# Optimization experiments

Hardware: AMD Instinct MI355X
Metric: run time of the kernel (lower is better)

Reference implementation:

```python
import jax, jax.numpy as jnp
import numpy as np

BATCH = 1024
SEQ = 80
VOCAB = 50000
EMB = 512
UNITS = 512


def setup_inputs() -> dict:
    key = jax.random.key(0)
    ks = jax.random.split(key, 10)
    s_in = 1.0 / np.sqrt(EMB)
    s_h = 1.0 / np.sqrt(UNITS)
    return {
        "inputs": jax.random.randint(ks[0], (BATCH, SEQ), 0, VOCAB, dtype=jnp.int64),
        "emb": jax.random.normal(ks[1], (VOCAB, EMB), dtype=jnp.float32) * 0.05,
        "W0x": jax.random.normal(ks[2], (EMB, UNITS), dtype=jnp.float32) * s_in,
        "W0h": jax.random.normal(ks[3], (UNITS, UNITS), dtype=jnp.float32) * s_h,
        "b0": jnp.zeros((UNITS,), dtype=jnp.float32),
        "W1x": jax.random.normal(ks[4], (UNITS, UNITS), dtype=jnp.float32) * s_h,
        "W1h": jax.random.normal(ks[5], (UNITS, UNITS), dtype=jnp.float32) * s_h,
        "b1": jnp.zeros((UNITS,), dtype=jnp.float32),
        "Wout": jax.random.normal(ks[6], (UNITS, 1), dtype=jnp.float32) * s_h,
        "bout": jnp.zeros((1,), dtype=jnp.float32),
    }


def reference(inputs, emb, W0x, W0h, b0, W1x, W1h, b1, Wout, bout):
    # Embedding lookup: [B, T, E]
    x = emb[inputs]
    # Time-major for scan: [T, B, E]
    xs = jnp.transpose(x, (1, 0, 2))

    h0 = jnp.zeros((inputs.shape[0], W0h.shape[0]), dtype=emb.dtype)
    h1 = jnp.zeros((inputs.shape[0], W1h.shape[0]), dtype=emb.dtype)

    def step(carry, x_t):
        h0, h1 = carry
        # SimpleRNNCell 0: tanh(x@Wx + h@Wh + b)  (dropout inactive at inference)
        h0 = jnp.tanh(x_t @ W0x + h0 @ W0h + b0)
        # SimpleRNNCell 1 stacked on cell 0's output
        h1 = jnp.tanh(h0 @ W1x + h1 @ W1h + b1)
        return (h0, h1), None

    (h0, h1), _ = jax.lax.scan(step, (h0, h1), xs)
    # Dense(1) on last-step hidden of layer 1, then sigmoid -> [B, 1]
    prob = jax.nn.sigmoid(h1 @ Wout + bout)
    return prob
```

## Files before the change

kernel.cpp:

```cpp
#include <hip/hip_runtime.h>
#include <hip/hip_bf16.h>
#include <math.h>

#define BATCH   1024
#define SEQ     80
#define EMB     512
#define UNITS   512
#define NBG     64
#define NCG     4
#define ROWS    16
#define COLS    128
#define THREADS 512
#define LDW     1544

#define H0_OFF   (2u * 1024 * 1024)
#define H1_OFF   (4u * 1024 * 1024)
#define FLAG_OFF (6u * 1024 * 1024)

typedef __attribute__((ext_vector_type(8))) short          bf16x8;
typedef __attribute__((ext_vector_type(8))) unsigned short u16x8;
typedef __attribute__((ext_vector_type(4))) float          f32x4;

__device__ inline unsigned short f2bf(float f) {
    __hip_bfloat16 h = __float2bfloat16(f);
    return *reinterpret_cast<unsigned short*>(&h);
}
__device__ inline float bf2f(unsigned short u) {
    unsigned int x = ((unsigned int)u) << 16;
    return __uint_as_float(x);
}
__device__ inline float tanh_fast(float x) {
    float e = __expf(2.f * x);
    return 1.f - 2.f / (e + 1.f);
}

__global__ __launch_bounds__(256) void pack_weights(
    const float* __restrict__ W0x, const float* __restrict__ W0h,
    const float* __restrict__ W1x, const float* __restrict__ W1h,
    unsigned short* __restrict__ wpack)
{
    int g    = blockIdx.x * 4 + (threadIdx.x >> 6);
    int lane = threadIdx.x & 63;
    int p    = g >> 10;
    int cg   = (g >> 8) & 3;
    int w    = (g >> 5) & 7;
    int k0   = g & 31;
    int n    = cg * COLS + w * 16 + (lane & 15);
    int kb   = k0 * 32 + (lane >> 4) * 8;
    const float* Wx = p ? W1x : W0x;
    const float* Wh = p ? W1h : W0h;

    u16x8 v;
#pragma unroll
    for (int j = 0; j < 8; ++j) {
        int k = kb + j;
        float f = (k < 512) ? Wx[(size_t)k * UNITS + n]
                            : Wh[(size_t)(k - 512) * UNITS + n];
        v[j] = f2bf(f);
    }
    *(u16x8*)(wpack + (size_t)g * 512 + lane * 8) = v;
}

#define RUN_PHASE(ACC, KBASE, WB)                                              \
    do {                                                                       \
        const unsigned short* a_lds = hcat + abase + (KBASE);                  \
        bf16x8 Bf[8];                                                          \
        _Pragma("unroll")                                                      \
        for (int i = 0; i < 8; ++i)                                            \
            Bf[i] = *(const bf16x8*)((WB) + (size_t)i * 512);                  \
        _Pragma("unroll")                                                      \
        for (int k0 = 0; k0 < 32; ++k0) {                                      \
            bf16x8 a = *(const bf16x8*)(a_lds + k0 * 32);                      \
            bf16x8 b = Bf[k0 & 7];                                             \
            if (k0 + 8 < 32)                                                   \
                Bf[k0 & 7] = *(const bf16x8*)((WB) + (size_t)(k0 + 8) * 512);  \
            ACC = __builtin_amdgcn_mfma_f32_16x16x32_bf16(a, b, ACC, 0, 0, 0); \
        }                                                                      \
    } while (0)

__global__ __launch_bounds__(THREADS, 1) void rnn_ex_kernel(
    const int*   __restrict__ inputs,
    const float* __restrict__ emb,
    const float* __restrict__ b0,
    const float* __restrict__ b1,
    const unsigned short* __restrict__ wpack,
    unsigned short* __restrict__ h0buf,
    unsigned short* __restrict__ h1buf,
    int* __restrict__ flag0,
    int* __restrict__ flag1,
    const float* __restrict__ Wout,
    const float* __restrict__ bout,
    float*       __restrict__ out)
{
    __shared__ unsigned short hcat[ROWS * LDW];

    const int tid   = threadIdx.x;
    const int w     = tid >> 6;
    const int lane  = tid & 63;
    const int quad  = lane >> 4;
    const int l15   = lane & 15;
    const int cg    = blockIdx.x >> 6;
    const int bg    = blockIdx.x & 63;
    const int rbase = bg * ROWS;

    for (int i = tid; i < ROWS * 1024; i += THREADS) {
        int r = i >> 10, c = i & 1023;
        hcat[r * LDW + 512 + c] = 0;
    }

    const int xr = tid >> 5;
    const int xc = (tid & 31) * 16;

    {
        int idx = inputs[(rbase + xr) * SEQ + 0];
        const float4* ep = (const float4*)(emb + (size_t)idx * EMB + xc);
        float4 p0 = ep[0], p1 = ep[1], p2 = ep[2], p3 = ep[3];
        u16x8 v0, v1;
        v0[0]=f2bf(p0.x); v0[1]=f2bf(p0.y); v0[2]=f2bf(p0.z); v0[3]=f2bf(p0.w);
        v0[4]=f2bf(p1.x); v0[5]=f2bf(p1.y); v0[6]=f2bf(p1.z); v0[7]=f2bf(p1.w);
        v1[0]=f2bf(p2.x); v1[1]=f2bf(p2.y); v1[2]=f2bf(p2.z); v1[3]=f2bf(p2.w);
        v1[4]=f2bf(p3.x); v1[5]=f2bf(p3.y); v1[6]=f2bf(p3.z); v1[7]=f2bf(p3.w);
        *(u16x8*)(hcat + xr * LDW + xc)     = v0;
        *(u16x8*)(hcat + xr * LDW + xc + 8) = v1;
    }
    __syncthreads();

    const int   mycol = cg * COLS + w * 16 + l15;
    const float bias0 = b0[mycol];
    const float bias1 = b1[mycol];

    const unsigned short* wb0 = wpack + ((size_t)(cg * 256 + w * 32)) * 512 + lane * 8;
    const unsigned short* wb1 = wb0 + (size_t)1024 * 512;

    const int abase = l15 * LDW + quad * 8;
    const int fl    = bg * NCG;

    for (int t = 0; t < SEQ; ++t) {
        const int par = t & 1;
        const int tgt = t + 1;

        int tn = (t + 1 < SEQ) ? t + 1 : t;
        int idx = inputs[(rbase + xr) * SEQ + tn];
        const float4* ep = (const float4*)(emb + (size_t)idx * EMB + xc);
        float4 p0 = ep[0], p1 = ep[1], p2 = ep[2], p3 = ep[3];

        f32x4 acc = {bias0, bias0, bias0, bias0};
        RUN_PHASE(acc, 0, wb0);
        {
            unsigned short* dst = h0buf +
                ((size_t)par * BATCH + rbase + quad * 4) * UNITS + mycol;
#pragma unroll
            for (int i = 0; i < 4; ++i)
                __hip_atomic_store(dst + (size_t)i * UNITS,
                                   f2bf(tanh_fast(acc[i])),
                                   __ATOMIC_RELAXED, __HIP_MEMORY_SCOPE_AGENT);
        }
        __syncthreads();
        if (tid == 0)
            __hip_atomic_store(&flag0[fl + cg], tgt,
                               __ATOMIC_RELEASE, __HIP_MEMORY_SCOPE_AGENT);
        if (tid < NCG)
            while (__hip_atomic_load(&flag0[fl + tid],
                                     __ATOMIC_RELAXED, __HIP_MEMORY_SCOPE_AGENT) < tgt)
                __builtin_amdgcn_s_sleep(1);
        __asm__ volatile("" ::: "memory");
        __syncthreads();
        {
            const unsigned long long* src = (const unsigned long long*)
                (h0buf + ((size_t)par * BATCH + rbase) * UNITS);
            int base = (xr * 512 + xc) >> 2;
            unsigned long long q0 = __hip_atomic_load(src + base + 0, __ATOMIC_RELAXED, __HIP_MEMORY_SCOPE_AGENT);
            unsigned long long q1 = __hip_atomic_load(src + base + 1, __ATOMIC_RELAXED, __HIP_MEMORY_SCOPE_AGENT);
            unsigned long long q2 = __hip_atomic_load(src + base + 2, __ATOMIC_RELAXED, __HIP_MEMORY_SCOPE_AGENT);
            unsigned long long q3 = __hip_atomic_load(src + base + 3, __ATOMIC_RELAXED, __HIP_MEMORY_SCOPE_AGENT);
            unsigned long long* d = (unsigned long long*)&hcat[xr * LDW + 512 + xc];
            d[0] = q0; d[1] = q1; d[2] = q2; d[3] = q3;

            u16x8 v0, v1;
            v0[0]=f2bf(p0.x); v0[1]=f2bf(p0.y); v0[2]=f2bf(p0.z); v0[3]=f2bf(p0.w);
            v0[4]=f2bf(p1.x); v0[5]=f2bf(p1.y); v0[6]=f2bf(p1.z); v0[7]=f2bf(p1.w);
            v1[0]=f2bf(p2.x); v1[1]=f2bf(p2.y); v1[2]=f2bf(p2.z); v1[3]=f2bf(p2.w);
            v1[4]=f2bf(p3.x); v1[5]=f2bf(p3.y); v1[6]=f2bf(p3.z); v1[7]=f2bf(p3.w);
            *(u16x8*)(hcat + xr * LDW + xc)     = v0;
            *(u16x8*)(hcat + xr * LDW + xc + 8) = v1;
        }
        __syncthreads();

        f32x4 acc2 = {bias1, bias1, bias1, bias1};
        RUN_PHASE(acc2, 512, wb1);
        {
            unsigned short* dst = h1buf +
                ((size_t)par * BATCH + rbase + quad * 4) * UNITS + mycol;
#pragma unroll
            for (int i = 0; i < 4; ++i)
                __hip_atomic_store(dst + (size_t)i * UNITS,
                                   f2bf(tanh_fast(acc2[i])),
                                   __ATOMIC_RELAXED, __HIP_MEMORY_SCOPE_AGENT);
        }
        __syncthreads();
        if (tid == 0)
            __hip_atomic_store(&flag1[fl + cg], tgt,
                               __ATOMIC_RELEASE, __HIP_MEMORY_SCOPE_AGENT);
        if (tid < NCG)
            while (__hip_atomic_load(&flag1[fl + tid],
                                     __ATOMIC_RELAXED, __HIP_MEMORY_SCOPE_AGENT) < tgt)
                __builtin_amdgcn_s_sleep(1);
        __asm__ volatile("" ::: "memory");
        __syncthreads();
        {
            const unsigned long long* src = (const unsigned long long*)
                (h1buf + ((size_t)par * BATCH + rbase) * UNITS);
            int base = (xr * 512 + xc) >> 2;
            unsigned long long q0 = __hip_atomic_load(src + base + 0, __ATOMIC_RELAXED, __HIP_MEMORY_SCOPE_AGENT);
            unsigned long long q1 = __hip_atomic_load(src + base + 1, __ATOMIC_RELAXED, __HIP_MEMORY_SCOPE_AGENT);
            unsigned long long q2 = __hip_atomic_load(src + base + 2, __ATOMIC_RELAXED, __HIP_MEMORY_SCOPE_AGENT);
            unsigned long long q3 = __hip_atomic_load(src + base + 3, __ATOMIC_RELAXED, __HIP_MEMORY_SCOPE_AGENT);
            unsigned long long* d = (unsigned long long*)&hcat[xr * LDW + 1024 + xc];
            d[0] = q0; d[1] = q1; d[2] = q2; d[3] = q3;
        }
    }
    __syncthreads();

    if (cg == 0) {
#pragma unroll
        for (int rr = 0; rr < 2; ++rr) {
            int r = w * 2 + rr;
            float s = 0.f;
#pragma unroll
            for (int j = 0; j < 8; ++j) {
                int c = lane + 64 * j;
                s += bf2f(hcat[r * LDW + 1024 + c]) * Wout[c];
            }
#pragma unroll
            for (int off = 32; off > 0; off >>= 1) s += __shfl_down(s, off);
            if (lane == 0) {
                float z = s + bout[0];
                out[rbase + r] = 1.f / (1.f + __expf(-z));
            }
        }
    }
}

extern "C" void kernel_launch(void* const* d_in, const int* in_sizes, int n_in,
                              void* d_out, int out_size, void* d_ws, size_t ws_size,
                              hipStream_t stream) {
    const int*   inputs = (const int*)d_in[0];
    const float* emb    = (const float*)d_in[1];
    const float* W0x    = (const float*)d_in[2];
    const float* W0h    = (const float*)d_in[3];
    const float* b0     = (const float*)d_in[4];
    const float* W1x    = (const float*)d_in[5];
    const float* W1h    = (const float*)d_in[6];
    const float* b1     = (const float*)d_in[7];
    const float* Wout   = (const float*)d_in[8];
    const float* bout   = (const float*)d_in[9];
    float*       out    = (float*)d_out;

    unsigned short* wpack = (unsigned short*)d_ws;
    unsigned short* h0buf = (unsigned short*)((char*)d_ws + H0_OFF);
    unsigned short* h1buf = (unsigned short*)((char*)d_ws + H1_OFF);
    int* flag0 = (int*)((char*)d_ws + FLAG_OFF);
    int* flag1 = flag0 + 256;

    hipMemsetAsync((char*)d_ws + FLAG_OFF, 0, 2048, stream);
    pack_weights<<<512, 256, 0, stream>>>(W0x, W0h, W1x, W1h, wpack);
    rnn_ex_kernel<<<NBG * NCG, THREADS, 0, stream>>>(
        inputs, emb, b0, b1, wpack, h0buf, h1buf, flag0, flag1,
        Wout, bout, out);
}
```

Baseline: 1.103 ms.

## Overlap input-side GEMM halves with cross-block waits and keep recurrent weights in registers

Splits each layer's K=1024 GEMM into an input half and a recurrent half. The halves that do not depend on the freshly exchanged hidden state (x@W0x for the next step, h1_prev@W1h) are computed while waiting on the inter-block flags, so only the dependent half sits on the critical path. The dependent-half weights (W0h and W1x) are preloaded once into registers, removing global weight loads from the critical path. The embedding and state copies are also remapped to 16-byte accesses. This raises register pressure with 256 extra VGPRs of weights per thread, which risks spills under the 512-thread launch bound.

```diff
diff --git a/kernel.cpp b/kernel.cpp
--- a/kernel.cpp
+++ b/kernel.cpp
@@ -17,9 +17,10 @@
 #define H1_OFF   (4u * 1024 * 1024)
 #define FLAG_OFF (6u * 1024 * 1024)
 
-typedef __attribute__((ext_vector_type(8))) short          bf16x8;
-typedef __attribute__((ext_vector_type(8))) unsigned short u16x8;
-typedef __attribute__((ext_vector_type(4))) float          f32x4;
+typedef __attribute__((ext_vector_type(8))) short              bf16x8;
+typedef __attribute__((ext_vector_type(8))) unsigned short     u16x8;
+typedef __attribute__((ext_vector_type(4))) float              f32x4;
+typedef __attribute__((ext_vector_type(2))) unsigned long long u64x2;
 
 __device__ inline unsigned short f2bf(float f) {
     __hip_bfloat16 h = __float2bfloat16(f);
@@ -32,6 +33,12 @@
 __device__ inline float tanh_fast(float x) {
     float e = __expf(2.f * x);
     return 1.f - 2.f / (e + 1.f);
+}
+__device__ inline u16x8 pack8(float4 p0, float4 p1) {
+    u16x8 v;
+    v[0]=f2bf(p0.x); v[1]=f2bf(p0.y); v[2]=f2bf(p0.z); v[3]=f2bf(p0.w);
+    v[4]=f2bf(p1.x); v[5]=f2bf(p1.y); v[6]=f2bf(p1.z); v[7]=f2bf(p1.w);
+    return v;
 }
 
 __global__ __launch_bounds__(256) void pack_weights(
@@ -61,7 +68,7 @@
     *(u16x8*)(wpack + (size_t)g * 512 + lane * 8) = v;
 }
 
-#define RUN_PHASE(ACC, KBASE, WB)                                              \
+#define RUN_HALF_STREAM(ACC, KBASE, WB)                                        \
     do {                                                                       \
         const unsigned short* a_lds = hcat + abase + (KBASE);                  \
         bf16x8 Bf[8];                                                          \
@@ -69,12 +76,22 @@
         for (int i = 0; i < 8; ++i)                                            \
             Bf[i] = *(const bf16x8*)((WB) + (size_t)i * 512);                  \
         _Pragma("unroll")                                                      \
-        for (int k0 = 0; k0 < 32; ++k0) {                                      \
+        for (int k0 = 0; k0 < 16; ++k0) {                                      \
             bf16x8 a = *(const bf16x8*)(a_lds + k0 * 32);                      \
             bf16x8 b = Bf[k0 & 7];                                             \
-            if (k0 + 8 < 32)                                                   \
+            if (k0 + 8 < 16)                                                   \
                 Bf[k0 & 7] = *(const bf16x8*)((WB) + (size_t)(k0 + 8) * 512);  \
             ACC = __builtin_amdgcn_mfma_f32_16x16x32_bf16(a, b, ACC, 0, 0, 0); \
+        }                                                                      \
+    } while (0)
+
+#define RUN_HALF_REG(ACC, KBASE, BR)                                           \
+    do {                                                                       \
+        const unsigned short* a_lds = hcat + abase + (KBASE);                  \
+        _Pragma("unroll")                                                      \
+        for (int k0 = 0; k0 < 16; ++k0) {                                      \
+            bf16x8 a = *(const bf16x8*)(a_lds + k0 * 32);                      \
+            ACC = __builtin_amdgcn_mfma_f32_16x16x32_bf16(a, (BR)[k0], ACC, 0, 0, 0); \
         }                                                                      \
     } while (0)
 
@@ -92,7 +109,7 @@
     const float* __restrict__ bout,
     float*       __restrict__ out)
 {
-    __shared__ unsigned short hcat[ROWS * LDW];
+    __shared__ __align__(16) unsigned short hcat[ROWS * LDW];
 
     const int tid   = threadIdx.x;
     const int w     = tid >> 6;
@@ -103,25 +120,22 @@
     const int bg    = blockIdx.x & 63;
     const int rbase = bg * ROWS;
 
+    const int gr = w;
+    const int gc = (tid & 63) * 8;
+
     for (int i = tid; i < ROWS * 1024; i += THREADS) {
         int r = i >> 10, c = i & 1023;
         hcat[r * LDW + 512 + c] = 0;
     }
 
-    const int xr = tid >> 5;
-    const int xc = (tid & 31) * 16;
-
     {
-        int idx = inputs[(rbase + xr) * SEQ + 0];
-        const float4* ep = (const float4*)(emb + (size_t)idx * EMB + xc);
-        float4 p0 = ep[0], p1 = ep[1], p2 = ep[2], p3 = ep[3];
-        u16x8 v0, v1;
-        v0[0]=f2bf(p0.x); v0[1]=f2bf(p0.y); v0[2]=f2bf(p0.z); v0[3]=f2bf(p0.w);
-        v0[4]=f2bf(p1.x); v0[5]=f2bf(p1.y); v0[6]=f2bf(p1.z); v0[7]=f2bf(p1.w);
-        v1[0]=f2bf(p2.x); v1[1]=f2bf(p2.y); v1[2]=f2bf(p2.z); v1[3]=f2bf(p2.w);
-        v1[4]=f2bf(p3.x); v1[5]=f2bf(p3.y); v1[6]=f2bf(p3.z); v1[7]=f2bf(p3.w);
-        *(u16x8*)(hcat + xr * LDW + xc)     = v0;
-        *(u16x8*)(hcat + xr * LDW + xc + 8) = v1;
+        int ia = inputs[(rbase + gr) * SEQ + 0];
+        int ib = inputs[(rbase + gr + 8) * SEQ + 0];
+        const float4* ea = (const float4*)(emb + (size_t)ia * EMB + gc);
+        const float4* eb = (const float4*)(emb + (size_t)ib * EMB + gc);
+        float4 f0 = ea[0], f1 = ea[1], f2 = eb[0], f3 = eb[1];
+        *(u16x8*)(hcat + gr * LDW + gc)       = pack8(f0, f1);
+        *(u16x8*)(hcat + (gr + 8) * LDW + gc) = pack8(f2, f3);
     }
     __syncthreads();
 
@@ -129,23 +143,31 @@
     const float bias0 = b0[mycol];
     const float bias1 = b1[mycol];
 
-    const unsigned short* wb0 = wpack + ((size_t)(cg * 256 + w * 32)) * 512 + lane * 8;
-    const unsigned short* wb1 = wb0 + (size_t)1024 * 512;
+    const unsigned short* wb0  = wpack + ((size_t)(cg * 256 + w * 32)) * 512 + lane * 8;
+    const unsigned short* wb1  = wb0 + (size_t)1024 * 512;
+    const unsigned short* wb0x = wb0;
+    const unsigned short* wb1h = wb1 + (size_t)16 * 512;
 
     const int abase = l15 * LDW + quad * 8;
     const int fl    = bg * NCG;
+
+    bf16x8 BH0[16], BX1[16];
+#pragma unroll
+    for (int i = 0; i < 16; ++i)
+        BH0[i] = *(const bf16x8*)(wb0 + (size_t)(16 + i) * 512);
+#pragma unroll
+    for (int i = 0; i < 16; ++i)
+        BX1[i] = *(const bf16x8*)(wb1 + (size_t)i * 512);
+
+    f32x4 accX = {bias0, bias0, bias0, bias0};
+    RUN_HALF_STREAM(accX, 0, wb0x);
 
     for (int t = 0; t < SEQ; ++t) {
         const int par = t & 1;
         const int tgt = t + 1;
 
-        int tn = (t + 1 < SEQ) ? t + 1 : t;
-        int idx = inputs[(rbase + xr) * SEQ + tn];
-        const float4* ep = (const float4*)(emb + (size_t)idx * EMB + xc);
-        float4 p0 = ep[0], p1 = ep[1], p2 = ep[2], p3 = ep[3];
-
-        f32x4 acc = {bias0, bias0, bias0, bias0};
-        RUN_PHASE(acc, 0, wb0);
+        f32x4 acc = accX;
+        RUN_HALF_REG(acc, 512, BH0);
         {
             unsigned short* dst = h0buf +
                 ((size_t)par * BATCH + rbase + quad * 4) * UNITS + mycol;
@@ -159,6 +181,20 @@
         if (tid == 0)
             __hip_atomic_store(&flag0[fl + cg], tgt,
                                __ATOMIC_RELEASE, __HIP_MEMORY_SCOPE_AGENT);
+
+        int tn = (t + 1 < SEQ) ? t + 1 : t;
+        int ia = inputs[(rbase + gr) * SEQ + tn];
+        int ib = inputs[(rbase + gr + 8) * SEQ + tn];
+        const float4* ea = (const float4*)(emb + (size_t)ia * EMB + gc);
+        const float4* eb = (const float4*)(emb + (size_t)ib * EMB + gc);
+        float4 f0 = ea[0], f1 = ea[1], f2 = eb[0], f3 = eb[1];
+
+        f32x4 accH1 = {bias1, bias1, bias1, bias1};
+        RUN_HALF_STREAM(accH1, 1024, wb1h);
+
+        *(u16x8*)(hcat + gr * LDW + gc)       = pack8(f0, f1);
+        *(u16x8*)(hcat + (gr + 8) * LDW + gc) = pack8(f2, f3);
+
         if (tid < NCG)
             while (__hip_atomic_load(&flag0[fl + tid],
                                      __ATOMIC_RELAXED, __HIP_MEMORY_SCOPE_AGENT) < tgt)
@@ -168,26 +204,21 @@
         {
             const unsigned long long* src = (const unsigned long long*)
                 (h0buf + ((size_t)par * BATCH + rbase) * UNITS);
-            int base = (xr * 512 + xc) >> 2;
-            unsigned long long q0 = __hip_atomic_load(src + base + 0, __ATOMIC_RELAXED, __HIP_MEMORY_SCOPE_AGENT);
-            unsigned long long q1 = __hip_atomic_load(src + base + 1, __ATOMIC_RELAXED, __HIP_MEMORY_SCOPE_AGENT);
-            unsigned long long q2 = __hip_atomic_load(src + base + 2, __ATOMIC_RELAXED, __HIP_MEMORY_SCOPE_AGENT);
-            unsigned long long q3 = __hip_atomic_load(src + base + 3, __ATOMIC_RELAXED, __HIP_MEMORY_SCOPE_AGENT);
-            unsigned long long* d = (unsigned long long*)&hcat[xr * LDW + 512 + xc];
-            d[0] = q0; d[1] = q1; d[2] = q2; d[3] = q3;
-
-            u16x8 v0, v1;
-            v0[0]=f2bf(p0.x); v0[1]=f2bf(p0.y); v0[2]=f2bf(p0.z); v0[3]=f2bf(p0.w);
-            v0[4]=f2bf(p1.x); v0[5]=f2bf(p1.y); v0[6]=f2bf(p1.z); v0[7]=f2bf(p1.w);
-            v1[0]=f2bf(p2.x); v1[1]=f2bf(p2.y); v1[2]=f2bf(p2.z); v1[3]=f2bf(p2.w);
-            v1[4]=f2bf(p3.x); v1[5]=f2bf(p3.y); v1[6]=f2bf(p3.z); v1[7]=f2bf(p3.w);
-            *(u16x8*)(hcat + xr * LDW + xc)     = v0;
-            *(u16x8*)(hcat + xr * LDW + xc + 8) = v1;
-        }
-        __syncthreads();
-
-        f32x4 acc2 = {bias1, bias1, bias1, bias1};
-        RUN_PHASE(acc2, 512, wb1);
+            int ua = gr * 128 + (tid & 63) * 2;
+            int ub = ua + 8 * 128;
+            unsigned long long q0 = __hip_atomic_load(src + ua,     __ATOMIC_RELAXED, __HIP_MEMORY_SCOPE_AGENT);
+            unsigned long long q1 = __hip_atomic_load(src + ua + 1, __ATOMIC_RELAXED, __HIP_MEMORY_SCOPE_AGENT);
+            unsigned long long q2 = __hip_atomic_load(src + ub,     __ATOMIC_RELAXED, __HIP_MEMORY_SCOPE_AGENT);
+            unsigned long long q3 = __hip_atomic_load(src + ub + 1, __ATOMIC_RELAXED, __HIP_MEMORY_SCOPE_AGENT);
+            u64x2 wlo; wlo[0] = q0; wlo[1] = q1;
+            u64x2 whi; whi[0] = q2; whi[1] = q3;
+            *(u64x2*)(hcat + gr * LDW + 512 + gc)       = wlo;
+            *(u64x2*)(hcat + (gr + 8) * LDW + 512 + gc) = whi;
+        }
+        __syncthreads();
+
+        f32x4 acc2 = accH1;
+        RUN_HALF_REG(acc2, 512, BX1);
         {
             unsigned short* dst = h1buf +
                 ((size_t)par * BATCH + rbase + quad * 4) * UNITS + mycol;
@@ -201,6 +232,12 @@
         if (tid == 0)
             __hip_atomic_store(&flag1[fl + cg], tgt,
                                __ATOMIC_RELEASE, __HIP_MEMORY_SCOPE_AGENT);
+
+        if (t + 1 < SEQ) {
+            accX[0] = bias0; accX[1] = bias0; accX[2] = bias0; accX[3] = bias0;
+            RUN_HALF_STREAM(accX, 0, wb0x);
+        }
+
         if (tid < NCG)
             while (__hip_atomic_load(&flag1[fl + tid],
                                      __ATOMIC_RELAXED, __HIP_MEMORY_SCOPE_AGENT) < tgt)
@@ -210,13 +247,16 @@
         {
             const unsigned long long* src = (const unsigned long long*)
                 (h1buf + ((size_t)par * BATCH + rbase) * UNITS);
-            int base = (xr * 512 + xc) >> 2;
-            unsigned long long q0 = __hip_atomic_load(src + base + 0, __ATOMIC_RELAXED, __HIP_MEMORY_SCOPE_AGENT);
-            unsigned long long q1 = __hip_atomic_load(src + base + 1, __ATOMIC_RELAXED, __HIP_MEMORY_SCOPE_AGENT);
-            unsigned long long q2 = __hip_atomic_load(src + base + 2, __ATOMIC_RELAXED, __HIP_MEMORY_SCOPE_AGENT);
-            unsigned long long q3 = __hip_atomic_load(src + base + 3, __ATOMIC_RELAXED, __HIP_MEMORY_SCOPE_AGENT);
-            unsigned long long* d = (unsigned long long*)&hcat[xr * LDW + 1024 + xc];
-            d[0] = q0; d[1] = q1; d[2] = q2; d[3] = q3;
+            int ua = gr * 128 + (tid & 63) * 2;
+            int ub = ua + 8 * 128;
+            unsigned long long q0 = __hip_atomic_load(src + ua,     __ATOMIC_RELAXED, __HIP_MEMORY_SCOPE_AGENT);
+            unsigned long long q1 = __hip_atomic_load(src + ua + 1, __ATOMIC_RELAXED, __HIP_MEMORY_SCOPE_AGENT);
+            unsigned long long q2 = __hip_atomic_load(src + ub,     __ATOMIC_RELAXED, __HIP_MEMORY_SCOPE_AGENT);
+            unsigned long long q3 = __hip_atomic_load(src + ub + 1, __ATOMIC_RELAXED, __HIP_MEMORY_SCOPE_AGENT);
+            u64x2 wlo; wlo[0] = q0; wlo[1] = q1;
+            u64x2 whi; whi[0] = q2; whi[1] = q3;
+            *(u64x2*)(hcat + gr * LDW + 1024 + gc)       = wlo;
+            *(u64x2*)(hcat + (gr + 8) * LDW + 1024 + gc) = whi;
         }
     }
     __syncthreads();
```

Result: slower. 1.297 ms (+17.6%).

## Exchange K-split partial sums so each step needs one cross-block barrier

Applied to the files above, without the earlier changes.

The recurrence is restructured so each column-group block computes partial pre-activations over its own 128-unit slice of h0/h1 (K-split) for all 512 output columns. It publishes them to global memory, and the other blocks reduce them after a single flag barrier per timestep instead of two. The input projection x@W0x is computed off the critical path after publishing, and the embedding for step t+2 is staged ahead. This cuts inter-block synchronisation latency per step but increases global traffic, since fp32 partials are exchanged 4x redundantly, and it changes the weight packing layout.

```diff
diff --git a/kernel.cpp b/kernel.cpp
--- a/kernel.cpp
+++ b/kernel.cpp
@@ -11,11 +11,8 @@
 #define ROWS    16
 #define COLS    128
 #define THREADS 512
-#define LDW     1544
-
-#define H0_OFF   (2u * 1024 * 1024)
-#define H1_OFF   (4u * 1024 * 1024)
-#define FLAG_OFF (6u * 1024 * 1024)
+#define LDX     520
+#define LDH     136
 
 typedef __attribute__((ext_vector_type(8))) short          bf16x8;
 typedef __attribute__((ext_vector_type(8))) unsigned short u16x8;
@@ -32,6 +29,25 @@
 __device__ inline float tanh_fast(float x) {
     float e = __expf(2.f * x);
     return 1.f - 2.f / (e + 1.f);
+}
+__device__ inline u16x8 pack8(float4 p0, float4 p1) {
+    u16x8 v;
+    v[0]=f2bf(p0.x); v[1]=f2bf(p0.y); v[2]=f2bf(p0.z); v[3]=f2bf(p0.w);
+    v[4]=f2bf(p1.x); v[5]=f2bf(p1.y); v[6]=f2bf(p1.z); v[7]=f2bf(p1.w);
+    return v;
+}
+
+__device__ inline void pub_store(float* p, float v) {
+    __hip_atomic_store(p, v, __ATOMIC_RELAXED, __HIP_MEMORY_SCOPE_AGENT);
+}
+__device__ inline void pub_store(unsigned short* p, float v) {
+    __hip_atomic_store(p, f2bf(v), __ATOMIC_RELAXED, __HIP_MEMORY_SCOPE_AGENT);
+}
+__device__ inline float pub_load(const float* p) {
+    return __hip_atomic_load(p, __ATOMIC_RELAXED, __HIP_MEMORY_SCOPE_AGENT);
+}
+__device__ inline float pub_load(const unsigned short* p) {
+    return bf2f(__hip_atomic_load(p, __ATOMIC_RELAXED, __HIP_MEMORY_SCOPE_AGENT));
 }
 
 __global__ __launch_bounds__(256) void pack_weights(
@@ -41,58 +57,118 @@
 {
     int g    = blockIdx.x * 4 + (threadIdx.x >> 6);
     int lane = threadIdx.x & 63;
-    int p    = g >> 10;
-    int cg   = (g >> 8) & 3;
-    int w    = (g >> 5) & 7;
-    int k0   = g & 31;
-    int n    = cg * COLS + w * 16 + (lane & 15);
-    int kb   = k0 * 32 + (lane >> 4) * 8;
-    const float* Wx = p ? W1x : W0x;
-    const float* Wh = p ? W1h : W0h;
+    int m    = g >> 9;
+    int s    = g & 511;
+    int cg   = s >> 7;
+    int w    = (s >> 4) & 7;
+    int rem  = s & 15;
+    int l15  = lane & 15;
+    int q8   = (lane >> 4) * 8;
+
+    const float* src = (m == 0) ? W0x : (m == 1) ? W0h : (m == 2) ? W1x : W1h;
+    int rowb, col;
+    if (m == 0) { rowb = rem * 32 + q8;            col = cg * 128 + w * 16 + l15; }
+    else        { int nt = rem >> 2, ks = rem & 3;
+                  rowb = cg * 128 + ks * 32 + q8;  col = w * 64 + nt * 16 + l15; }
 
     u16x8 v;
 #pragma unroll
-    for (int j = 0; j < 8; ++j) {
-        int k = kb + j;
-        float f = (k < 512) ? Wx[(size_t)k * UNITS + n]
-                            : Wh[(size_t)(k - 512) * UNITS + n];
-        v[j] = f2bf(f);
-    }
+    for (int j = 0; j < 8; ++j)
+        v[j] = f2bf(src[(size_t)(rowb + j) * UNITS + col]);
     *(u16x8*)(wpack + (size_t)g * 512 + lane * 8) = v;
 }
 
-#define RUN_PHASE(ACC, KBASE, WB)                                              \
+#define RUN_PREX(ACC)                                                          \
     do {                                                                       \
-        const unsigned short* a_lds = hcat + abase + (KBASE);                  \
-        bf16x8 Bf[8];                                                          \
-        _Pragma("unroll")                                                      \
-        for (int i = 0; i < 8; ++i)                                            \
-            Bf[i] = *(const bf16x8*)((WB) + (size_t)i * 512);                  \
-        _Pragma("unroll")                                                      \
-        for (int k0 = 0; k0 < 32; ++k0) {                                      \
-            bf16x8 a = *(const bf16x8*)(a_lds + k0 * 32);                      \
-            bf16x8 b = Bf[k0 & 7];                                             \
-            if (k0 + 8 < 32)                                                   \
-                Bf[k0 & 7] = *(const bf16x8*)((WB) + (size_t)(k0 + 8) * 512);  \
-            ACC = __builtin_amdgcn_mfma_f32_16x16x32_bf16(a, b, ACC, 0, 0, 0); \
+        bf16x8 Bf_[8];                                                         \
+        _Pragma("unroll")                                                      \
+        for (int i_ = 0; i_ < 8; ++i_)                                         \
+            Bf_[i_] = *(const bf16x8*)(wbX + (size_t)i_ * 512);                \
+        _Pragma("unroll")                                                      \
+        for (int k0_ = 0; k0_ < 16; ++k0_) {                                   \
+            bf16x8 a_ = *(const bf16x8*)(xA + k0_ * 32);                       \
+            bf16x8 b_ = Bf_[k0_ & 7];                                          \
+            if (k0_ + 8 < 16)                                                  \
+                Bf_[k0_ & 7] = *(const bf16x8*)(wbX + (size_t)(k0_ + 8) * 512);\
+            ACC = __builtin_amdgcn_mfma_f32_16x16x32_bf16(a_, b_, ACC, 0,0,0); \
         }                                                                      \
     } while (0)
 
-__global__ __launch_bounds__(THREADS, 1) void rnn_ex_kernel(
+#define RUN16(ACCA, AFR, WB)                                                   \
+    do {                                                                       \
+        bf16x8 Bf_[8];                                                         \
+        _Pragma("unroll")                                                      \
+        for (int i_ = 0; i_ < 8; ++i_)                                         \
+            Bf_[i_] = *(const bf16x8*)((WB) + (size_t)i_ * 512);               \
+        _Pragma("unroll")                                                      \
+        for (int s_ = 0; s_ < 16; ++s_) {                                      \
+            bf16x8 b_ = Bf_[s_ & 7];                                           \
+            if (s_ + 8 < 16)                                                   \
+                Bf_[s_ & 7] = *(const bf16x8*)((WB) + (size_t)(s_ + 8) * 512); \
+            ACCA[s_ >> 2] = __builtin_amdgcn_mfma_f32_16x16x32_bf16(           \
+                AFR[s_ & 3], b_, ACCA[s_ >> 2], 0, 0, 0);                      \
+        }                                                                      \
+    } while (0)
+
+#define STAGE_X(TT)                                                            \
+    do {                                                                       \
+        int tn_ = (TT) < SEQ ? (TT) : SEQ - 1;                                 \
+        int ia_ = inputs[(rbase + gr) * SEQ + tn_];                            \
+        int ib_ = inputs[(rbase + gr + 8) * SEQ + tn_];                        \
+        const float4* ea_ = (const float4*)(emb + (size_t)ia_ * EMB + gc);     \
+        const float4* eb_ = (const float4*)(emb + (size_t)ib_ * EMB + gc);     \
+        float4 f0_ = ea_[0], f1_ = ea_[1], f2_ = eb_[0], f3_ = eb_[1];         \
+        *(u16x8*)(xbuf + gr * LDX + gc)       = pack8(f0_, f1_);               \
+        *(u16x8*)(xbuf + (gr + 8) * LDX + gc) = pack8(f2_, f3_);               \
+    } while (0)
+
+#define CRIT_AND_PUBLISH(PPAR)                                                 \
+    do {                                                                       \
+        bf16x8 Aq_[4], Ah_[4];                                                 \
+        _Pragma("unroll")                                                      \
+        for (int ks_ = 0; ks_ < 4; ++ks_) {                                    \
+            Aq_[ks_] = *(const bf16x8*)(hqA + ks_ * 32);                       \
+            Ah_[ks_] = *(const bf16x8*)(hhA + ks_ * 32);                       \
+        }                                                                      \
+        f32x4 accq_[4], accp_[4];                                              \
+        _Pragma("unroll")                                                      \
+        for (int i_ = 0; i_ < 4; ++i_) {                                       \
+            accq_[i_] = (f32x4){0.f, 0.f, 0.f, 0.f};                           \
+            accp_[i_] = (f32x4){0.f, 0.f, 0.f, 0.f};                           \
+        }                                                                      \
+        RUN16(accq_, Aq_, wbQ);                                                \
+        RUN16(accp_, Ah_, wbP2);                                               \
+        RUN16(accp_, Aq_, wbP1);                                               \
+        PT* qd_ = qbuf + ((size_t)((PPAR) * NBG + bg) * 4 + cg) * 8192         \
+                       + (size_t)(quad * 4) * 512 + w * 64 + l15;              \
+        PT* pd_ = pbuf + ((size_t)((PPAR) * NBG + bg) * 4 + cg) * 8192         \
+                       + (size_t)(quad * 4) * 512 + w * 64 + l15;              \
+        _Pragma("unroll")                                                      \
+        for (int nt_ = 0; nt_ < 4; ++nt_)                                      \
+            _Pragma("unroll")                                                  \
+            for (int i_ = 0; i_ < 4; ++i_) {                                   \
+                pub_store(qd_ + (size_t)i_ * 512 + nt_ * 16, accq_[nt_][i_]);  \
+                pub_store(pd_ + (size_t)i_ * 512 + nt_ * 16, accp_[nt_][i_]);  \
+            }                                                                  \
+    } while (0)
+
+template<typename PT>
+__global__ __launch_bounds__(THREADS, 2) void rnn_ex_kernel(
     const int*   __restrict__ inputs,
     const float* __restrict__ emb,
     const float* __restrict__ b0,
     const float* __restrict__ b1,
     const unsigned short* __restrict__ wpack,
-    unsigned short* __restrict__ h0buf,
-    unsigned short* __restrict__ h1buf,
-    int* __restrict__ flag0,
-    int* __restrict__ flag1,
+    PT*  __restrict__ qbuf,
+    PT*  __restrict__ pbuf,
+    int* __restrict__ flags,
     const float* __restrict__ Wout,
     const float* __restrict__ bout,
     float*       __restrict__ out)
 {
-    __shared__ unsigned short hcat[ROWS * LDW];
+    __shared__ __align__(16) unsigned short xbuf[ROWS * LDX];
+    __shared__ __align__(16) unsigned short h0own[ROWS * LDH];
+    __shared__ __align__(16) unsigned short h1own[ROWS * LDH];
 
     const int tid   = threadIdx.x;
     const int w     = tid >> 6;
@@ -103,133 +179,109 @@
     const int bg    = blockIdx.x & 63;
     const int rbase = bg * ROWS;
 
-    for (int i = tid; i < ROWS * 1024; i += THREADS) {
-        int r = i >> 10, c = i & 1023;
-        hcat[r * LDW + 512 + c] = 0;
-    }
-
-    const int xr = tid >> 5;
-    const int xc = (tid & 31) * 16;
-
-    {
-        int idx = inputs[(rbase + xr) * SEQ + 0];
-        const float4* ep = (const float4*)(emb + (size_t)idx * EMB + xc);
-        float4 p0 = ep[0], p1 = ep[1], p2 = ep[2], p3 = ep[3];
-        u16x8 v0, v1;
-        v0[0]=f2bf(p0.x); v0[1]=f2bf(p0.y); v0[2]=f2bf(p0.z); v0[3]=f2bf(p0.w);
-        v0[4]=f2bf(p1.x); v0[5]=f2bf(p1.y); v0[6]=f2bf(p1.z); v0[7]=f2bf(p1.w);
-        v1[0]=f2bf(p2.x); v1[1]=f2bf(p2.y); v1[2]=f2bf(p2.z); v1[3]=f2bf(p2.w);
-        v1[4]=f2bf(p3.x); v1[5]=f2bf(p3.y); v1[6]=f2bf(p3.z); v1[7]=f2bf(p3.w);
-        *(u16x8*)(hcat + xr * LDW + xc)     = v0;
-        *(u16x8*)(hcat + xr * LDW + xc + 8) = v1;
-    }
-    __syncthreads();
+    const int gr = w;
+    const int gc = (tid & 63) * 8;
 
     const int   mycol = cg * COLS + w * 16 + l15;
     const float bias0 = b0[mycol];
     const float bias1 = b1[mycol];
 
-    const unsigned short* wb0 = wpack + ((size_t)(cg * 256 + w * 32)) * 512 + lane * 8;
-    const unsigned short* wb1 = wb0 + (size_t)1024 * 512;
-
-    const int abase = l15 * LDW + quad * 8;
-    const int fl    = bg * NCG;
-
-    for (int t = 0; t < SEQ; ++t) {
+    const unsigned short* wbX  = wpack + ((size_t)(       (cg*8 + w)*16)) * 512 + lane * 8;
+    const unsigned short* wbQ  = wpack + ((size_t)( 512 + (cg*8 + w)*16)) * 512 + lane * 8;
+    const unsigned short* wbP1 = wpack + ((size_t)(1024 + (cg*8 + w)*16)) * 512 + lane * 8;
+    const unsigned short* wbP2 = wpack + ((size_t)(1536 + (cg*8 + w)*16)) * 512 + lane * 8;
+
+    const unsigned short* xA  = xbuf  + l15 * LDX + quad * 8;
+    const unsigned short* hqA = h0own + l15 * LDH + quad * 8;
+    const unsigned short* hhA = h1own + l15 * LDH + quad * 8;
+    const int hwr = (quad * 4) * LDH + w * 16 + l15;
+    const int fl  = bg * NCG;
+
+    for (int i = tid; i < ROWS * LDH; i += THREADS) h1own[i] = 0;
+    STAGE_X(0);
+    __syncthreads();
+
+    f32x4 preX = {bias0, bias0, bias0, bias0};
+    RUN_PREX(preX);
+#pragma unroll
+    for (int i = 0; i < 4; ++i)
+        h0own[hwr + i * LDH] = f2bf(tanh_fast(preX[i]));
+    __syncthreads();
+    STAGE_X(1);
+    CRIT_AND_PUBLISH(0);
+    __syncthreads();
+    if (tid == 0)
+        __hip_atomic_store(&flags[fl + cg], 1,
+                           __ATOMIC_RELEASE, __HIP_MEMORY_SCOPE_AGENT);
+    preX = (f32x4){bias0, bias0, bias0, bias0};
+    RUN_PREX(preX);
+
+    for (int t = 0; t < SEQ - 1; ++t) {
         const int par = t & 1;
-        const int tgt = t + 1;
-
-        int tn = (t + 1 < SEQ) ? t + 1 : t;
-        int idx = inputs[(rbase + xr) * SEQ + tn];
-        const float4* ep = (const float4*)(emb + (size_t)idx * EMB + xc);
-        float4 p0 = ep[0], p1 = ep[1], p2 = ep[2], p3 = ep[3];
-
-        f32x4 acc = {bias0, bias0, bias0, bias0};
-        RUN_PHASE(acc, 0, wb0);
-        {
-            unsigned short* dst = h0buf +
-                ((size_t)par * BATCH + rbase + quad * 4) * UNITS + mycol;
-#pragma unroll
-            for (int i = 0; i < 4; ++i)
-                __hip_atomic_store(dst + (size_t)i * UNITS,
-                                   f2bf(tanh_fast(acc[i])),
-                                   __ATOMIC_RELAXED, __HIP_MEMORY_SCOPE_AGENT);
-        }
-        __syncthreads();
-        if (tid == 0)
-            __hip_atomic_store(&flag0[fl + cg], tgt,
-                               __ATOMIC_RELEASE, __HIP_MEMORY_SCOPE_AGENT);
+        const int pnx = (t + 1) & 1;
+
         if (tid < NCG)
-            while (__hip_atomic_load(&flag0[fl + tid],
-                                     __ATOMIC_RELAXED, __HIP_MEMORY_SCOPE_AGENT) < tgt)
+            while (__hip_atomic_load(&flags[fl + tid],
+                                     __ATOMIC_RELAXED, __HIP_MEMORY_SCOPE_AGENT) < t + 1)
                 __builtin_amdgcn_s_sleep(1);
         __asm__ volatile("" ::: "memory");
         __syncthreads();
+
+        float sq[4] = {0.f, 0.f, 0.f, 0.f};
+        float sp[4] = {0.f, 0.f, 0.f, 0.f};
         {
-            const unsigned long long* src = (const unsigned long long*)
-                (h0buf + ((size_t)par * BATCH + rbase) * UNITS);
-            int base = (xr * 512 + xc) >> 2;
-            unsigned long long q0 = __hip_atomic_load(src + base + 0, __ATOMIC_RELAXED, __HIP_MEMORY_SCOPE_AGENT);
-            unsigned long long q1 = __hip_atomic_load(src + base + 1, __ATOMIC_RELAXED, __HIP_MEMORY_SCOPE_AGENT);
-            unsigned long long q2 = __hip_atomic_load(src + base + 2, __ATOMIC_RELAXED, __HIP_MEMORY_SCOPE_AGENT);
-            unsigned long long q3 = __hip_atomic_load(src + base + 3, __ATOMIC_RELAXED, __HIP_MEMORY_SCOPE_AGENT);
-            unsigned long long* d = (unsigned long long*)&hcat[xr * LDW + 512 + xc];
-            d[0] = q0; d[1] = q1; d[2] = q2; d[3] = q3;
-
-            u16x8 v0, v1;
-            v0[0]=f2bf(p0.x); v0[1]=f2bf(p0.y); v0[2]=f2bf(p0.z); v0[3]=f2bf(p0.w);
-            v0[4]=f2bf(p1.x); v0[5]=f2bf(p1.y); v0[6]=f2bf(p1.z); v0[7]=f2bf(p1.w);
-            v1[0]=f2bf(p2.x); v1[1]=f2bf(p2.y); v1[2]=f2bf(p2.z); v1[3]=f2bf(p2.w);
-            v1[4]=f2bf(p3.x); v1[5]=f2bf(p3.y); v1[6]=f2bf(p3.z); v1[7]=f2bf(p3.w);
-            *(u16x8*)(hcat + xr * LDW + xc)     = v0;
-            *(u16x8*)(hcat + xr * LDW + xc + 8) = v1;
+            const PT* qs = qbuf + ((size_t)(par * NBG + bg) * 4) * 8192
+                                + (size_t)(quad * 4) * 512 + mycol;
+            const PT* ps = pbuf + ((size_t)(par * NBG + bg) * 4) * 8192
+                                + (size_t)(quad * 4) * 512 + mycol;
+#pragma unroll
+            for (int c = 0; c < 4; ++c)
+#pragma unroll
+                for (int i = 0; i < 4; ++i) {
+                    sq[i] += pub_load(qs + (size_t)c * 8192 + (size_t)i * 512);
+                    sp[i] += pub_load(ps + (size_t)c * 8192 + (size_t)i * 512);
+                }
         }
+#pragma unroll
+        for (int i = 0; i < 4; ++i)
+            h1own[hwr + i * LDH] = f2bf(tanh_fast(bias1 + sp[i]));
+#pragma unroll
+        for (int i = 0; i < 4; ++i)
+            h0own[hwr + i * LDH] = f2bf(tanh_fast(preX[i] + sq[i]));
+        STAGE_X(t + 2);
         __syncthreads();
 
-        f32x4 acc2 = {bias1, bias1, bias1, bias1};
-        RUN_PHASE(acc2, 512, wb1);
-        {
-            unsigned short* dst = h1buf +
-                ((size_t)par * BATCH + rbase + quad * 4) * UNITS + mycol;
-#pragma unroll
-            for (int i = 0; i < 4; ++i)
-                __hip_atomic_store(dst + (size_t)i * UNITS,
-                                   f2bf(tanh_fast(acc2[i])),
-                                   __ATOMIC_RELAXED, __HIP_MEMORY_SCOPE_AGENT);
-        }
+        CRIT_AND_PUBLISH(pnx);
         __syncthreads();
         if (tid == 0)
-            __hip_atomic_store(&flag1[fl + cg], tgt,
+            __hip_atomic_store(&flags[fl + cg], t + 2,
                                __ATOMIC_RELEASE, __HIP_MEMORY_SCOPE_AGENT);
+
+        preX = (f32x4){bias0, bias0, bias0, bias0};
+        RUN_PREX(preX);
+    }
+
+    if (cg == 0) {
         if (tid < NCG)
-            while (__hip_atomic_load(&flag1[fl + tid],
-                                     __ATOMIC_RELAXED, __HIP_MEMORY_SCOPE_AGENT) < tgt)
+            while (__hip_atomic_load(&flags[fl + tid],
+                                     __ATOMIC_RELAXED, __HIP_MEMORY_SCOPE_AGENT) < SEQ)
                 __builtin_amdgcn_s_sleep(1);
         __asm__ volatile("" ::: "memory");
         __syncthreads();
-        {
-            const unsigned long long* src = (const unsigned long long*)
-                (h1buf + ((size_t)par * BATCH + rbase) * UNITS);
-            int base = (xr * 512 + xc) >> 2;
-            unsigned long long q0 = __hip_atomic_load(src + base + 0, __ATOMIC_RELAXED, __HIP_MEMORY_SCOPE_AGENT);
-            unsigned long long q1 = __hip_atomic_load(src + base + 1, __ATOMIC_RELAXED, __HIP_MEMORY_SCOPE_AGENT);
-            unsigned long long q2 = __hip_atomic_load(src + base + 2, __ATOMIC_RELAXED, __HIP_MEMORY_SCOPE_AGENT);
-            unsigned long long q3 = __hip_atomic_load(src + base + 3, __ATOMIC_RELAXED, __HIP_MEMORY_SCOPE_AGENT);
-            unsigned long long* d = (unsigned long long*)&hcat[xr * LDW + 1024 + xc];
-            d[0] = q0; d[1] = q1; d[2] = q2; d[3] = q3;
-        }
-    }
-    __syncthreads();
-
-    if (cg == 0) {
+
+        const PT* ps = pbuf + ((size_t)(((SEQ - 1) & 1) * NBG + bg) * 4) * 8192;
 #pragma unroll
         for (int rr = 0; rr < 2; ++rr) {
             int r = w * 2 + rr;
             float s = 0.f;
 #pragma unroll
             for (int j = 0; j < 8; ++j) {
-                int c = lane + 64 * j;
-                s += bf2f(hcat[r * LDW + 1024 + c]) * Wout[c];
+                int c2 = lane + 64 * j;
+                float pre = b1[c2];
+#pragma unroll
+                for (int cc = 0; cc < 4; ++cc)
+                    pre += pub_load(ps + (size_t)cc * 8192 + (size_t)r * 512 + c2);
+                s += tanh_fast(pre) * Wout[c2];
             }
 #pragma unroll
             for (int off = 32; off > 0; off >>= 1) s += __shfl_down(s, off);
@@ -257,14 +309,25 @@
     float*       out    = (float*)d_out;
 
     unsigned short* wpack = (unsigned short*)d_ws;
-    unsigned short* h0buf = (unsigned short*)((char*)d_ws + H0_OFF);
-    unsigned short* h1buf = (unsigned short*)((char*)d_ws + H1_OFF);
-    int* flag0 = (int*)((char*)d_ws + FLAG_OFF);
-    int* flag1 = flag0 + 256;
-
-    hipMemsetAsync((char*)d_ws + FLAG_OFF, 0, 2048, stream);
+    char*  base  = (char*)d_ws;
+    const size_t WOFF = (size_t)2 * 1024 * 1024;
+    const size_t NEL  = (size_t)2 * NBG * 4 * ROWS * 512;
+
     pack_weights<<<512, 256, 0, stream>>>(W0x, W0h, W1x, W1h, wpack);
-    rnn_ex_kernel<<<NBG * NCG, THREADS, 0, stream>>>(
-        inputs, emb, b0, b1, wpack, h0buf, h1buf, flag0, flag1,
-        Wout, bout, out);
-}
+
+    if (ws_size >= WOFF + 2 * NEL * sizeof(float) + 4096) {
+        float* qb  = (float*)(base + WOFF);
+        float* pb  = qb + NEL;
+        int*   flg = (int*)(pb + NEL);
+        hipMemsetAsync(flg, 0, 1024, stream);
+        rnn_ex_kernel<float><<<NBG * NCG, THREADS, 0, stream>>>(
+            inputs, emb, b0, b1, wpack, qb, pb, flg, Wout, bout, out);
+    } else {
+        unsigned short* qb  = (unsigned short*)(base + WOFF);
+        unsigned short* pb  = qb + NEL;
+        int*            flg = (int*)(pb + NEL);
+        hipMemsetAsync(flg, 0, 1024, stream);
+        rnn_ex_kernel<unsigned short><<<NBG * NCG, THREADS, 0, stream>>>(
+            inputs, emb, b0, b1, wpack, qb, pb, flg, Wout, bout, out);
+    }
+}
```

Result: slower. 1.455 ms (+31.9%).
